# Performance work log

Measured on AMD Instinct MI355X. Metric: run time of the kernel, lower is better.

## Reference

```python
import jax, jax.numpy as jnp
import numpy as np

C = 1.0          # curvature args.c
ALPHA = 3.0      # self.alpha
MIN = 1e-15      # min_norm clamp (HGCN PoincareBall)
PROJ_EPS = 4e-3  # fp32 boundary eps (HGCN)


def _norm(x):
    return jnp.maximum(jnp.linalg.norm(x, axis=-1, keepdims=True), MIN)


def artanh(x):
    # clamp for fp32 stability (HGCN clamps to 1 - 1e-15; 1e-7 is the fp32 analogue)
    return jnp.arctanh(jnp.clip(x, -1.0 + 1e-7, 1.0 - 1e-7))


def proj(x, c):
    n = _norm(x)
    maxn = (1.0 - PROJ_EPS) / jnp.sqrt(c)
    return jnp.where(n > maxn, x / n * maxn, x)


def expmap0(u, c):
    sc = jnp.sqrt(c)
    n = _norm(u)
    return jnp.tanh(sc * n) * u / (sc * n)


def logmap0(p, c):
    sc = jnp.sqrt(c)
    n = _norm(p)
    return artanh(sc * n) * p / (sc * n)


def mobius_add(x, y, c):
    x2 = jnp.sum(x * x, axis=-1, keepdims=True)
    y2 = jnp.sum(y * y, axis=-1, keepdims=True)
    xy = jnp.sum(x * y, axis=-1, keepdims=True)
    num = (1.0 + 2.0 * c * xy + c * y2) * x + (1.0 - c * x2) * y
    den = 1.0 + 2.0 * c * xy + c * c * x2 * y2
    return num / jnp.maximum(den, MIN)


def mobius_matvec(m, x, c):
    sc = jnp.sqrt(c)
    xn = _norm(x)
    mx = x @ m.T                      # [..., out]
    mxn = _norm(mx)
    res = jnp.tanh(mxn / xn * artanh(sc * xn)) * mx / (mxn * sc)
    zero_rows = jnp.all(mx == 0.0, axis=-1, keepdims=True)
    return jnp.where(zero_rows, 0.0, res)


def hyp_linear(x, W, b, c):
    # dropout on weights is identity in eval mode
    mv = proj(mobius_matvec(W, x, c), c)
    hb = proj(expmap0(b[None, :], c), c)  # proj_tan0 is identity on Poincare ball
    return proj(mobius_add(mv, hb, c), c)


def setup_inputs() -> dict:
    key = jax.random.key(0)
    N, D, F = 8192, 128, 128
    ks = jax.random.split(key, 8)
    gain = np.sqrt(2.0 / (D + D)) * np.sqrt(2.0)  # xavier-like scale
    return {
        "idx": jnp.arange(N, dtype=jnp.int32),
        "dist_metrix": jnp.zeros((1,), dtype=jnp.float32),
        "x": jax.random.normal(ks[0], (N, F), dtype=jnp.float32),
        "emb1": jax.random.normal(ks[1], (N, D), dtype=jnp.float32),
        "emb2": jax.random.normal(ks[2], (N, D), dtype=jnp.float32),
        "W1": jax.random.normal(ks[3], (D, D), dtype=jnp.float32) * gain,
        "b1": jax.random.normal(ks[4], (D,), dtype=jnp.float32) * 0.01,
        "W2": jax.random.normal(ks[5], (D, D), dtype=jnp.float32) * gain,
        "b2": jax.random.normal(ks[6], (D,), dtype=jnp.float32) * 0.01,
    }


def reference(idx, dist_metrix, x, emb1, emb2, W1, b1, W2, b2):
    # node embeddings lifted to the Poincare ball (proj_tan0 is identity)
    nv1 = proj(expmap0(emb1[idx], C), C)
    nv2 = proj(expmap0(emb2[idx], C), C)
    nv1 = hyp_linear(nv1, W1, b1, C)
    nv2 = hyp_linear(nv2, W2, b2, C)
    # adjacency construction: a1 = nv2 @ nv1^T (mobius), a2 = nv1 @ nv2^T (mobius)
    a1 = mobius_matvec(nv1, nv2, C)   # [N, N]
    a2 = mobius_matvec(nv2, nv1, C)   # [N, N]
    a = mobius_add(a1, -a2, C)
    adj = jax.nn.relu(jnp.tanh(ALPHA * a))
    n = adj.shape[0]
    adj = adj + 1e-4 * jnp.eye(n, dtype=adj.dtype)
    # row-normalize (scipy round-trip in original == row-sum divide, inf -> 0)
    rs = jnp.sum(adj, axis=1, keepdims=True)
    adj = adj * jnp.where(rs == 0.0, 0.0, 1.0 / rs)
    # propagate features
    xt = logmap0(x, C)                       # [N, F]
    out = mobius_matvec(xt.T, adj, C)        # adj @ xt -> [N, F]
    out = logmap0(out, C)
    return out
```

## Files before the change

kernel.cpp:

```cpp
#include <hip/hip_runtime.h>
#include <hip/hip_bf16.h>


typedef __attribute__((ext_vector_type(8))) short short8;
typedef __attribute__((ext_vector_type(4))) float f32x4;

#define MAXN 0.996f

__device__ __forceinline__ float artanh_clip(float x) {
    x = fminf(x, 1.0f - 1e-7f);
    x = fmaxf(x, -1.0f + 1e-7f);
    return 0.5f * logf((1.0f + x) / (1.0f - x));
}

__device__ __forceinline__ float red8(float v) {
    v += __shfl_xor(v, 1);
    v += __shfl_xor(v, 2);
    v += __shfl_xor(v, 4);
    return v;
}

__device__ __forceinline__ float red64(float v) {
#pragma unroll
    for (int m = 1; m < 64; m <<= 1) v += __shfl_xor(v, m);
    return v;
}

__device__ __forceinline__ unsigned short f2bf(float f) {
    __hip_bfloat16 h = __float2bfloat16(f);
    return *reinterpret_cast<unsigned short*>(&h);
}

__device__ __forceinline__ float bf2f(unsigned short u) {
    __hip_bfloat16 h;
    *reinterpret_cast<unsigned short*>(&h) = u;
    return __bfloat162float(h);
}

__global__ __launch_bounds__(256) void prep_kernel(
    const int* __restrict__ idx, const float* __restrict__ x,
    const float* __restrict__ emb1, const float* __restrict__ emb2,
    const float* __restrict__ W1, const float* __restrict__ W2,
    const float* __restrict__ b1, const float* __restrict__ b2,
    unsigned short* __restrict__ nv1b, unsigned short* __restrict__ nv2b,
    unsigned short* __restrict__ xtT,
    float* __restrict__ xn1, float* __restrict__ xn2) {
    const int which = blockIdx.y;
    const int tid = threadIdx.x;
    const int rblk = blockIdx.x * 32;

    if (which == 2) {
        __shared__ float xv[32 * 132];
        const int r = tid >> 3, s = tid & 7;
        float ev[16];
        float p2 = 0.f;
#pragma unroll
        for (int kk = 0; kk < 16; ++kk) {
            float e = x[(rblk + r) * 128 + s + kk * 8];
            ev[kk] = e;
            p2 += e * e;
        }
        const float n = fmaxf(sqrtf(red8(p2)), 1e-15f);
        const float scl = artanh_clip(n) / n;
#pragma unroll
        for (int kk = 0; kk < 16; ++kk) xv[r * 132 + s + kk * 8] = ev[kk] * scl;
        __syncthreads();
        const int k = tid >> 1, h = tid & 1;
        short8 o0, o1;
#pragma unroll
        for (int j = 0; j < 8; ++j) o0[j] = (short)f2bf(xv[(h * 16 + j) * 132 + k]);
#pragma unroll
        for (int j = 0; j < 8; ++j) o1[j] = (short)f2bf(xv[(h * 16 + 8 + j) * 132 + k]);
        *reinterpret_cast<short8*>(&xtT[k * 8192 + rblk + h * 16]) = o0;
        *reinterpret_cast<short8*>(&xtT[k * 8192 + rblk + h * 16 + 8]) = o1;
        return;
    }

    __shared__ __align__(16) float uL[32 * 132];
    __shared__ float mxL[32 * 132];
    __shared__ float xnL[32];
    __shared__ float hbL[128];
    __shared__ float s2s[4];

    const float* emb = which ? emb2 : emb1;
    const float* W = which ? W2 : W1;
    const float* b = which ? b2 : b1;
    unsigned short* nvb = which ? nv2b : nv1b;
    float* xno = which ? xn2 : xn1;

    float bv = (tid < 128) ? b[tid] : 0.f;
    float ssq = red64(bv * bv);
    if ((tid & 63) == 0) s2s[tid >> 6] = ssq;
    __syncthreads();
    const float bn = fmaxf(sqrtf(s2s[0] + s2s[1]), 1e-15f);
    const float bth = tanhf(bn);
    const float bnu = fmaxf(bth, 1e-15f);
    const float bps = (bnu > MAXN) ? (MAXN / bnu) : 1.0f;
    if (tid < 128) hbL[tid] = bv * (bth / bn) * bps;
    const float hbn = fminf(bnu, MAXN);
    const float y2 = hbn * hbn;

    const int r = tid >> 3, s = tid & 7;
    const int row = rblk + r;
    const int src = idx[row];
    float ev[16];
    float p2 = 0.f;
#pragma unroll
    for (int kk = 0; kk < 16; ++kk) {
        float e = emb[src * 128 + s + kk * 8];
        ev[kk] = e;
        p2 += e * e;
    }
    float n2 = red8(p2);
    float n = fmaxf(sqrtf(n2), 1e-15f);
    float th = tanhf(n);
    float nu = fmaxf(th, 1e-15f);
    float ps = (nu > MAXN) ? (MAXN / nu) : 1.0f;
    float sc0 = (th / n) * ps;
#pragma unroll
    for (int kk = 0; kk < 16; ++kk) uL[r * 132 + s + kk * 8] = ev[kk] * sc0;
    if (s == 0) xnL[r] = fmaxf(nu * ps, 1e-15f);
    __syncthreads();

    const int o = tid & 127, rb = tid >> 7;
    float mxv[16];
#pragma unroll
    for (int rr = 0; rr < 16; ++rr) mxv[rr] = 0.f;
    for (int k4 = 0; k4 < 128; k4 += 4) {
        const float4 wv = *reinterpret_cast<const float4*>(&W[o * 128 + k4]);
#pragma unroll
        for (int rr = 0; rr < 16; ++rr) {
            const float4 uv = *reinterpret_cast<const float4*>(&uL[(rb + rr * 2) * 132 + k4]);
            mxv[rr] += uv.x * wv.x + uv.y * wv.y + uv.z * wv.z + uv.w * wv.w;
        }
    }
#pragma unroll
    for (int rr = 0; rr < 16; ++rr) mxL[(rb + rr * 2) * 132 + o] = mxv[rr];
    __syncthreads();

    float mx[16];
    float m2 = 0.f;
#pragma unroll
    for (int kk = 0; kk < 16; ++kk) {
        mx[kk] = mxL[r * 132 + s + kk * 8];
        m2 += mx[kk] * mx[kk];
    }
    float mxn = fmaxf(sqrtf(red8(m2)), 1e-15f);
    float xnv = xnL[r];
    float tt = tanhf(mxn / xnv * artanh_clip(xnv));
    float nres = fmaxf(tt, 1e-15f);
    float ps2 = (nres > MAXN) ? (MAXN / nres) : 1.0f;
    float s2 = (tt / mxn) * ps2;
    float mvn = nres * ps2;
    float x2 = mvn * mvn;
    float xyp = 0.f;
    float mv[16];
#pragma unroll
    for (int kk = 0; kk < 16; ++kk) {
        mv[kk] = mx[kk] * s2;
        xyp += mv[kk] * hbL[s + kk * 8];
    }
    float xy = red8(xyp);
    float cA = 1.f + 2.f * xy + y2;
    float cB = 1.f - x2;
    float rden = 1.f / fmaxf(1.f + 2.f * xy + x2 * y2, 1e-15f);
    float r2v[16];
    float q2 = 0.f;
#pragma unroll
    for (int kk = 0; kk < 16; ++kk) {
        float v = (cA * mv[kk] + cB * hbL[s + kk * 8]) * rden;
        r2v[kk] = v;
        q2 += v * v;
    }
    float nr2 = fmaxf(sqrtf(red8(q2)), 1e-15f);
    float ps3 = (nr2 > MAXN) ? (MAXN / nr2) : 1.0f;
#pragma unroll
    for (int kk = 0; kk < 16; ++kk) nvb[row * 128 + s + kk * 8] = f2bf(r2v[kk] * ps3);
    if (s == 0) xno[row] = fmaxf((nr2 > MAXN) ? MAXN : nr2, 1e-15f);
}

__global__ __launch_bounds__(256) void gram_kernel(const unsigned short* __restrict__ nv1b,
                                                   const unsigned short* __restrict__ nv2b,
                                                   float* __restrict__ G) {
    __shared__ float Ab[64 * 33], Bb[64 * 33];
    const int tile = blockIdx.x, mat = blockIdx.y, kc = blockIdx.z;
    const int ta = (tile & 3) * 32, tb = (tile >> 2) * 32;
    const unsigned short* Am = (mat == 1) ? nv2b : nv1b;
    const unsigned short* Bm = (mat == 0) ? nv1b : nv2b;
    const int tid = threadIdx.x;
    const int oa = tid & 31, obb = (tid >> 5) * 4;
    float acc[4] = {0.f, 0.f, 0.f, 0.f};
    for (int sc = 0; sc < 16; ++sc) {
        const int r0 = kc * 1024 + sc * 64;
        for (int i0 = tid; i0 < 2048; i0 += 256) {
            int rr = i0 >> 5, cc = i0 & 31;
            Ab[rr * 33 + cc] = bf2f(Am[(r0 + rr) * 128 + ta + cc]);
            Bb[rr * 33 + cc] = bf2f(Bm[(r0 + rr) * 128 + tb + cc]);
        }
        __syncthreads();
#pragma unroll 4
        for (int rr = 0; rr < 64; ++rr) {
            float av = Ab[rr * 33 + oa];
#pragma unroll
            for (int i = 0; i < 4; ++i) acc[i] += av * Bb[rr * 33 + obb + i];
        }
        __syncthreads();
    }
#pragma unroll
    for (int i = 0; i < 4; ++i)
        atomicAdd(&G[mat * 16384 + (ta + oa) * 128 + tb + obb + i], acc[i]);
}

__global__ __launch_bounds__(256) void rowcoef_kernel(
    const float* __restrict__ G, const float* __restrict__ xn1, const float* __restrict__ xn2,
    const unsigned short* __restrict__ nv1b, const unsigned short* __restrict__ nv2b,
    float* __restrict__ P, float* __restrict__ Q, float* __restrict__ Ad) {
    __shared__ __align__(16) float v1L[32 * 132];
    __shared__ __align__(16) float v2L[32 * 132];
    __shared__ float tL[32 * 132];
    __shared__ float RCX[3][32];
    __shared__ float dL[32];
    const int tid = threadIdx.x;
    const int rblk = blockIdx.x * 32;
    for (int i = tid; i < 4096; i += 256) {
        int r = i >> 7, c = i & 127;
        v1L[r * 132 + c] = bf2f(nv1b[(rblk + r) * 128 + c]);
        v2L[r * 132 + c] = bf2f(nv2b[(rblk + r) * 128 + c]);
    }
    __syncthreads();
    const int o = tid & 127, rb = tid >> 7;
    const int rA = tid >> 3, sA = tid & 7;
    for (int mat = 0; mat < 3; ++mat) {
        const float* vR = (mat == 0) ? v2L : v1L;
        const float* vL = (mat == 1) ? v1L : v2L;
        const float* Gm = G + mat * 16384;
        float tv[16];
#pragma unroll
        for (int rr = 0; rr < 16; ++rr) tv[rr] = 0.f;
        for (int k4 = 0; k4 < 128; k4 += 4) {
            const float4 gv = *reinterpret_cast<const float4*>(&Gm[o * 128 + k4]);
#pragma unroll
            for (int rr = 0; rr < 16; ++rr) {
                const float4 uv = *reinterpret_cast<const float4*>(&vR[(rb + rr * 2) * 132 + k4]);
                tv[rr] += uv.x * gv.x + uv.y * gv.y + uv.z * gv.z + uv.w * gv.w;
            }
        }
        __syncthreads();
#pragma unroll
        for (int rr = 0; rr < 16; ++rr) {
            int rw = rb + rr * 2;
            tL[rw * 132 + o] = vL[rw * 132 + o] * tv[rr];
        }
        __syncthreads();
        float p = 0.f;
#pragma unroll
        for (int kk = 0; kk < 16; ++kk) p += tL[rA * 132 + sA + kk * 8];
        p = red8(p);
        if (sA == 0) RCX[mat][rA] = p;
    }
    float dp = 0.f;
#pragma unroll
    for (int kk = 0; kk < 16; ++kk)
        dp += v1L[rA * 132 + sA + kk * 8] * v2L[rA * 132 + sA + kk * 8];
    dp = red8(dp);
    if (sA == 0) dL[rA] = dp;
    __syncthreads();
    if (tid < 32) {
        const int row = rblk + tid;
        const float R = RCX[0][tid], Cc = RCX[1][tid], X = RCX[2][tid];
        const float xn1v = xn1[row], xn2v = xn2[row];
        const float mxn1 = fmaxf(sqrtf(fmaxf(R, 0.f)), 1e-15f);
        const float t1 = tanhf(mxn1 / xn2v * artanh_clip(xn2v));
        const float f1 = t1 / mxn1;
        const float mxn2 = fmaxf(sqrtf(fmaxf(Cc, 0.f)), 1e-15f);
        const float t2 = tanhf(mxn2 / xn1v * artanh_clip(xn1v));
        const float f2 = t2 / mxn2;
        const float x2 = f1 * f1 * R, y2 = f2 * f2 * Cc;
        const float xy = -f1 * f2 * X;
        const float rden = 1.f / fmaxf(1.f + 2.f * xy + x2 * y2, 1e-15f);
        const float Pv = (1.f + 2.f * xy + y2) * f1 * rden;
        const float Qv = -(1.f - x2) * f2 * rden;
        P[row] = Pv;
        Q[row] = Qv;
        Ad[row] = fmaxf(tanhf(3.f * (Pv + Qv) * dL[tid]), 0.f);
    }
}

__global__ __launch_bounds__(512) void fused_kernel(
    const unsigned short* __restrict__ nv1b, const unsigned short* __restrict__ nv2b,
    const unsigned short* __restrict__ xtT,
    const float* __restrict__ P, const float* __restrict__ Q,
    const float* __restrict__ Ad,
    float* __restrict__ out) {
    __shared__ float UL[32 * 132];
    __shared__ float rsL[32], qL[32];

    const int tid = threadIdx.x;
    const int w = tid >> 6, l = tid & 63;
    const int g = l >> 4, c = l & 15;
    const int i0 = blockIdx.x * 32;

    for (int i = tid; i < 32 * 132; i += 512) UL[i] = 0.f;
    if (tid < 32) { rsL[tid] = 0.f; qL[tid] = 0.f; }
    __syncthreads();

    const float Pv0 = P[i0 + c], Pv1 = P[i0 + 16 + c];
    const float Qv0 = Q[i0 + c], Qv1 = Q[i0 + 16 + c];
    const bool needS2 = __any((fabsf(Qv0) > 1e-6f) || (fabsf(Qv1) > 1e-6f)) != 0;

    short8 Bn0[4], Bn1[4];
#pragma unroll
    for (int kk = 0; kk < 4; ++kk) {
        Bn0[kk] = *reinterpret_cast<const short8*>(nv2b + (i0 + c) * 128 + kk * 32 + g * 8);
        Bn1[kk] = *reinterpret_cast<const short8*>(nv2b + (i0 + 16 + c) * 128 + kk * 32 + g * 8);
    }

    const f32x4 z4 = {0.f, 0.f, 0.f, 0.f};
    f32x4 accU0[8], accU1[8];
#pragma unroll
    for (int ft = 0; ft < 8; ++ft) { accU0[ft] = z4; accU1[ft] = z4; }
    float rs0 = 0.f, rs1 = 0.f, q0 = 0.f, q1 = 0.f;

    const int aoff = (8 * (c >> 2) + (c & 3)) * 128 + g * 8;
    const size_t xoff = (size_t)c * 8192 + g * 8;

    auto elem = [&](float s, float s2v, float Pv, float Qv,
                    float& rsa, float& qa) -> float {
        float a = Pv * s;
        if (needS2) a = fmaf(Qv, s2v, a);
        float e = __builtin_amdgcn_exp2f(a * 8.65617025f);
        float t = 1.0f - 2.0f * __builtin_amdgcn_rcpf(e + 1.0f);
        float ad = fmaxf(t, 0.0f);
        rsa += ad;
        qa = fmaf(ad, ad, qa);
        return ad;
    };
    auto pack8 = [](const float* ad) -> short8 {
        union { unsigned u[4]; short8 s; } r;
#pragma unroll
        for (int k = 0; k < 4; ++k)
            r.u[k] = (unsigned)f2bf(ad[2 * k]) | ((unsigned)f2bf(ad[2 * k + 1]) << 16);
        return r.s;
    };

    short8 A0c[4], A1c[4];
    {
        const unsigned short* pa0 = nv1b + (size_t)(w * 32) * 128;
#pragma unroll
        for (int kk = 0; kk < 4; ++kk) {
            A0c[kk] = *reinterpret_cast<const short8*>(pa0 + aoff + kk * 32);
            A1c[kk] = *reinterpret_cast<const short8*>(pa0 + aoff + 512 + kk * 32);
        }
    }

    for (int t = 0; t < 32; ++t) {
        const int jb = (w + 8 * t) * 32;
        const int jbn = (w + 8 * ((t + 1) & 31)) * 32;

        short8 XB[8];
#pragma unroll
        for (int ft = 0; ft < 8; ++ft)
            XB[ft] = *reinterpret_cast<const short8*>(xtT + (size_t)ft * 16 * 8192 + xoff + jb);
        short8 A0n[4], A1n[4];
        {
            const unsigned short* pan = nv1b + (size_t)jbn * 128;
#pragma unroll
            for (int kk = 0; kk < 4; ++kk) {
                A0n[kk] = *reinterpret_cast<const short8*>(pan + aoff + kk * 32);
                A1n[kk] = *reinterpret_cast<const short8*>(pan + aoff + 512 + kk * 32);
            }
        }

        f32x4 s00 = z4, s10 = z4, s01 = z4, s11 = z4;
#pragma unroll
        for (int kk = 0; kk < 4; ++kk) {
            s00 = __builtin_amdgcn_mfma_f32_16x16x32_bf16(A0c[kk], Bn0[kk], s00, 0, 0, 0);
            s10 = __builtin_amdgcn_mfma_f32_16x16x32_bf16(A1c[kk], Bn0[kk], s10, 0, 0, 0);
            s01 = __builtin_amdgcn_mfma_f32_16x16x32_bf16(A0c[kk], Bn1[kk], s01, 0, 0, 0);
            s11 = __builtin_amdgcn_mfma_f32_16x16x32_bf16(A1c[kk], Bn1[kk], s11, 0, 0, 0);
        }
        f32x4 r00 = z4, r10 = z4, r01 = z4, r11 = z4;
        if (needS2) {
            const unsigned short* pa2 = nv2b + (size_t)jb * 128;
            short8 C0[4], C1[4], D0[4], D1[4];
#pragma unroll
            for (int kk = 0; kk < 4; ++kk) {
                C0[kk] = *reinterpret_cast<const short8*>(pa2 + aoff + kk * 32);
                C1[kk] = *reinterpret_cast<const short8*>(pa2 + aoff + 512 + kk * 32);
                D0[kk] = *reinterpret_cast<const short8*>(nv1b + (i0 + c) * 128 + kk * 32 + g * 8);
                D1[kk] = *reinterpret_cast<const short8*>(nv1b + (i0 + 16 + c) * 128 + kk * 32 + g * 8);
            }
#pragma unroll
            for (int kk = 0; kk < 4; ++kk) {
                r00 = __builtin_amdgcn_mfma_f32_16x16x32_bf16(C0[kk], D0[kk], r00, 0, 0, 0);
                r10 = __builtin_amdgcn_mfma_f32_16x16x32_bf16(C1[kk], D0[kk], r10, 0, 0, 0);
                r01 = __builtin_amdgcn_mfma_f32_16x16x32_bf16(C0[kk], D1[kk], r01, 0, 0, 0);
                r11 = __builtin_amdgcn_mfma_f32_16x16x32_bf16(C1[kk], D1[kk], r11, 0, 0, 0);
            }
        }

        float ad0[8], ad1[8];
#pragma unroll
        for (int v = 0; v < 4; ++v) {
            ad0[v]     = elem(s00[v], r00[v], Pv0, Qv0, rs0, q0);
            ad0[4 + v] = elem(s10[v], r10[v], Pv0, Qv0, rs0, q0);
            ad1[v]     = elem(s01[v], r01[v], Pv1, Qv1, rs1, q1);
            ad1[4 + v] = elem(s11[v], r11[v], Pv1, Qv1, rs1, q1);
        }
        const short8 af0 = pack8(ad0);
        const short8 af1 = pack8(ad1);
#pragma unroll
        for (int ft = 0; ft < 8; ++ft) {
            accU0[ft] = __builtin_amdgcn_mfma_f32_16x16x32_bf16(af0, XB[ft], accU0[ft], 0, 0, 0);
            accU1[ft] = __builtin_amdgcn_mfma_f32_16x16x32_bf16(af1, XB[ft], accU1[ft], 0, 0, 0);
        }
#pragma unroll
        for (int kk = 0; kk < 4; ++kk) { A0c[kk] = A0n[kk]; A1c[kk] = A1n[kk]; }
    }

    rs0 += __shfl_xor(rs0, 16); rs0 += __shfl_xor(rs0, 32);
    rs1 += __shfl_xor(rs1, 16); rs1 += __shfl_xor(rs1, 32);
    q0 += __shfl_xor(q0, 16);   q0 += __shfl_xor(q0, 32);
    q1 += __shfl_xor(q1, 16);   q1 += __shfl_xor(q1, 32);
    if (l < 16) {
        atomicAdd(&rsL[c], rs0);
        atomicAdd(&qL[c], q0);
        atomicAdd(&rsL[16 + c], rs1);
        atomicAdd(&qL[16 + c], q1);
    }
#pragma unroll
    for (int ftx = 0; ftx < 8; ++ftx) {
        const int ft = (ftx + w) & 7;
#pragma unroll
        for (int v = 0; v < 4; ++v) {
            atomicAdd(&UL[(4 * g + v) * 132 + ft * 16 + c], accU0[ft][v]);
            atomicAdd(&UL[(16 + 4 * g + v) * 132 + ft * 16 + c], accU1[ft][v]);
        }
    }
    __syncthreads();

    const int r = tid >> 4, cc = tid & 15;
    const float adg = Ad[i0 + r];
    const float rsv = rsL[r] + 1e-4f;
    const float wv = 1.f / rsv;
    float m[8];
    float m2 = 0.f;
#pragma unroll
    for (int e = 0; e < 8; ++e) {
        const float xv = bf2f(xtT[(size_t)(cc * 8 + e) * 8192 + i0 + r]);
        m[e] = (UL[r * 132 + cc * 8 + e] + 1e-4f * xv) * wv;
        m2 = fmaf(m[e], m[e], m2);
    }
    m2 += __shfl_xor(m2, 1);
    m2 += __shfl_xor(m2, 2);
    m2 += __shfl_xor(m2, 4);
    m2 += __shfl_xor(m2, 8);
    const float mxn = fmaxf(sqrtf(m2), 1e-15f);
    const float qv = fmaxf(qL[r] + 2e-4f * adg + 1e-8f, 0.f);
    const float xn = fmaxf(sqrtf(qv) * wv, 1e-15f);
    const float tt = tanhf(mxn / xn * artanh_clip(xn));
    const float nres = fmaxf(tt, 1e-15f);
    const float lsc = (tt / mxn) * (artanh_clip(nres) / nres);
    float4 o0 = {m[0] * lsc, m[1] * lsc, m[2] * lsc, m[3] * lsc};
    float4 o1 = {m[4] * lsc, m[5] * lsc, m[6] * lsc, m[7] * lsc};
    *reinterpret_cast<float4*>(out + (i0 + r) * 128 + cc * 8) = o0;
    *reinterpret_cast<float4*>(out + (i0 + r) * 128 + cc * 8 + 4) = o1;
}

extern "C" void kernel_launch(void* const* d_in, const int* in_sizes, int n_in,
                              void* d_out, int out_size, void* d_ws, size_t ws_size,
                              hipStream_t stream) {
    const int* idx = (const int*)d_in[0];
    const float* x = (const float*)d_in[2];
    const float* emb1 = (const float*)d_in[3];
    const float* emb2 = (const float*)d_in[4];
    const float* W1 = (const float*)d_in[5];
    const float* b1 = (const float*)d_in[6];
    const float* W2 = (const float*)d_in[7];
    const float* b2 = (const float*)d_in[8];
    float* out = (float*)d_out;
    char* ws = (char*)d_ws;

    unsigned short* nv1b = (unsigned short*)(ws + 0x000000);
    unsigned short* nv2b = (unsigned short*)(ws + 0x200000);
    unsigned short* xtT = (unsigned short*)(ws + 0x400000);
    float* G = (float*)(ws + 0x600000);
    float* xn1 = (float*)(ws + 0x630000);
    float* xn2 = (float*)(ws + 0x638000);
    float* P = (float*)(ws + 0x640000);
    float* Q = (float*)(ws + 0x648000);
    float* Ad = (float*)(ws + 0x650000);

    hipMemsetAsync(G, 0, 3 * 128 * 128 * sizeof(float), stream);
    prep_kernel<<<dim3(256, 3), 256, 0, stream>>>(idx, x, emb1, emb2, W1, W2, b1, b2,
                                                  nv1b, nv2b, xtT, xn1, xn2);
    gram_kernel<<<dim3(16, 3, 8), 256, 0, stream>>>(nv1b, nv2b, G);
    rowcoef_kernel<<<256, 256, 0, stream>>>(G, xn1, xn2, nv1b, nv2b, P, Q, Ad);
    fused_kernel<<<256, 512, 0, stream>>>(nv1b, nv2b, xtT, P, Q, Ad, out);
    (void)in_sizes; (void)n_in; (void)out_size; (void)ws_size; (void)d_in;
}
```

Before: 334.6 us.

## Split fused kernel column range across two blocks with global reduction and finalize pass

Each 32-row tile of the fused adjacency/propagation kernel is now handled by two blocks, each covering half of the column range. This doubles the grid from 256 to 512 blocks so more of the GPU's compute units have work. Partial U results are accumulated into the output buffer with global atomics, and row sums are written per half. A new finalize kernel then applies normalization and the logmap. The cost is an extra memset, global atomic traffic, one more launch, and out being used in place for the U accumulation.

```diff
diff --git a/kernel.cpp b/kernel.cpp
--- a/kernel.cpp
+++ b/kernel.cpp
@@ -286,19 +286,19 @@
     }
 }
 
-__global__ __launch_bounds__(512) void fused_kernel(
+__global__ __launch_bounds__(512, 4) void fused_kernel(
     const unsigned short* __restrict__ nv1b, const unsigned short* __restrict__ nv2b,
     const unsigned short* __restrict__ xtT,
     const float* __restrict__ P, const float* __restrict__ Q,
-    const float* __restrict__ Ad,
-    float* __restrict__ out) {
+    float* __restrict__ U, float* __restrict__ rsp, float* __restrict__ qsp) {
     __shared__ float UL[32 * 132];
     __shared__ float rsL[32], qL[32];
 
     const int tid = threadIdx.x;
     const int w = tid >> 6, l = tid & 63;
     const int g = l >> 4, c = l & 15;
-    const int i0 = blockIdx.x * 32;
+    const int i0 = (blockIdx.x >> 1) * 32;
+    const int jh = blockIdx.x & 1;
 
     for (int i = tid; i < 32 * 132; i += 512) UL[i] = 0.f;
     if (tid < 32) { rsL[tid] = 0.f; qL[tid] = 0.f; }
@@ -345,7 +345,7 @@
 
     short8 A0c[4], A1c[4];
     {
-        const unsigned short* pa0 = nv1b + (size_t)(w * 32) * 128;
+        const unsigned short* pa0 = nv1b + (size_t)((w + 8 * (16 * jh)) * 32) * 128;
 #pragma unroll
         for (int kk = 0; kk < 4; ++kk) {
             A0c[kk] = *reinterpret_cast<const short8*>(pa0 + aoff + kk * 32);
@@ -353,9 +353,9 @@
         }
     }
 
-    for (int t = 0; t < 32; ++t) {
-        const int jb = (w + 8 * t) * 32;
-        const int jbn = (w + 8 * ((t + 1) & 31)) * 32;
+    for (int t = 0; t < 16; ++t) {
+        const int jb = (w + 8 * (16 * jh + t)) * 32;
+        const int jbn = (w + 8 * (16 * jh + ((t + 1) & 15))) * 32;
 
         short8 XB[8];
 #pragma unroll
@@ -439,32 +439,37 @@
     }
     __syncthreads();
 
-    const int r = tid >> 4, cc = tid & 15;
-    const float adg = Ad[i0 + r];
-    const float rsv = rsL[r] + 1e-4f;
+    for (int i = tid; i < 32 * 128; i += 512) {
+        const int r = i >> 7, cc = i & 127;
+        atomicAdd(&U[(i0 + r) * 128 + cc], UL[r * 132 + cc]);
+    }
+    if (tid < 32) {
+        rsp[jh * 8192 + i0 + tid] = rsL[tid];
+        qsp[jh * 8192 + i0 + tid] = qL[tid];
+    }
+}
+
+__global__ __launch_bounds__(256) void finalize_kernel(
+    const float* __restrict__ U, const float* __restrict__ rsp,
+    const float* __restrict__ qsp, const float* __restrict__ Ad,
+    const unsigned short* __restrict__ xtT, float* __restrict__ out) {
+    const int tid = threadIdx.x;
+    const int row = blockIdx.x * 4 + (tid >> 6);
+    const int l = tid & 63;
+    const float rsv = rsp[row] + rsp[8192 + row] + 1e-4f;
+    const float qv = fmaxf(qsp[row] + qsp[8192 + row] + 2e-4f * Ad[row] + 1e-8f, 0.f);
     const float wv = 1.f / rsv;
-    float m[8];
-    float m2 = 0.f;
-#pragma unroll
-    for (int e = 0; e < 8; ++e) {
-        const float xv = bf2f(xtT[(size_t)(cc * 8 + e) * 8192 + i0 + r]);
-        m[e] = (UL[r * 132 + cc * 8 + e] + 1e-4f * xv) * wv;
-        m2 = fmaf(m[e], m[e], m2);
-    }
-    m2 += __shfl_xor(m2, 1);
-    m2 += __shfl_xor(m2, 2);
-    m2 += __shfl_xor(m2, 4);
-    m2 += __shfl_xor(m2, 8);
-    const float mxn = fmaxf(sqrtf(m2), 1e-15f);
-    const float qv = fmaxf(qL[r] + 2e-4f * adg + 1e-8f, 0.f);
+    const float xv0 = bf2f(xtT[(size_t)l * 8192 + row]);
+    const float xv1 = bf2f(xtT[(size_t)(l + 64) * 8192 + row]);
+    const float m0 = (U[row * 128 + l] + 1e-4f * xv0) * wv;
+    const float m1 = (U[row * 128 + 64 + l] + 1e-4f * xv1) * wv;
+    const float mxn = fmaxf(sqrtf(red64(m0 * m0 + m1 * m1)), 1e-15f);
     const float xn = fmaxf(sqrtf(qv) * wv, 1e-15f);
     const float tt = tanhf(mxn / xn * artanh_clip(xn));
     const float nres = fmaxf(tt, 1e-15f);
     const float lsc = (tt / mxn) * (artanh_clip(nres) / nres);
-    float4 o0 = {m[0] * lsc, m[1] * lsc, m[2] * lsc, m[3] * lsc};
-    float4 o1 = {m[4] * lsc, m[5] * lsc, m[6] * lsc, m[7] * lsc};
-    *reinterpret_cast<float4*>(out + (i0 + r) * 128 + cc * 8) = o0;
-    *reinterpret_cast<float4*>(out + (i0 + r) * 128 + cc * 8 + 4) = o1;
+    out[row * 128 + l] = m0 * lsc;
+    out[row * 128 + 64 + l] = m1 * lsc;
 }
 
 extern "C" void kernel_launch(void* const* d_in, const int* in_sizes, int n_in,
@@ -490,12 +495,17 @@
     float* P = (float*)(ws + 0x640000);
     float* Q = (float*)(ws + 0x648000);
     float* Ad = (float*)(ws + 0x650000);
+    float* rsp = (float*)(ws + 0x660000);
+    float* qsp = (float*)(ws + 0x670000);
+    float* U = out;
 
     hipMemsetAsync(G, 0, 3 * 128 * 128 * sizeof(float), stream);
+    hipMemsetAsync(U, 0, 8192 * 128 * sizeof(float), stream);
     prep_kernel<<<dim3(256, 3), 256, 0, stream>>>(idx, x, emb1, emb2, W1, W2, b1, b2,
                                                   nv1b, nv2b, xtT, xn1, xn2);
     gram_kernel<<<dim3(16, 3, 8), 256, 0, stream>>>(nv1b, nv2b, G);
     rowcoef_kernel<<<256, 256, 0, stream>>>(G, xn1, xn2, nv1b, nv2b, P, Q, Ad);
-    fused_kernel<<<256, 512, 0, stream>>>(nv1b, nv2b, xtT, P, Q, Ad, out);
+    fused_kernel<<<512, 512, 0, stream>>>(nv1b, nv2b, xtT, P, Q, U, rsp, qsp);
+    finalize_kernel<<<2048, 256, 0, stream>>>(U, rsp, qsp, Ad, xtT, out);
     (void)in_sizes; (void)n_in; (void)out_size; (void)ws_size; (void)d_in;
 }
```

Result: slower. 657.9 us (+96.6%).
